# Kernel tuning notes

Measured on AMD Instinct MI355X. Metric: run time of the kernel, lower is better.

Reference implementation:

```python
import jax, jax.numpy as jnp
import numpy as np

N, E, B = 50000, 600000, 64
C_IN, H, C_OUT, L = 128, 128, 64, 3
BN_EPS = 1e-5


def setup_inputs() -> dict:
    key = jax.random.key(0)
    ks = iter(jax.random.split(key, 40))

    def w(shape, fan_in):
        return jax.random.normal(next(ks), shape, jnp.float32) / np.sqrt(fan_in).astype(np.float32)

    return {
        "x": jax.random.normal(next(ks), (N, C_IN), jnp.float32),
        "edge_index": jax.random.randint(next(ks), (2, E), 0, N),
        "batch": jnp.sort(jax.random.randint(next(ks), (N,), 0, B)),
        # GINConv MLPs: Linear(in,h) -> BN -> ReLU -> Linear(h,h)   (stacked over L; C_IN == H)
        "convW1": w((L, C_IN, H), C_IN), "convb1": jnp.zeros((L, H), jnp.float32),
        "bn_g": jnp.ones((L, H), jnp.float32), "bn_b": jnp.zeros((L, H), jnp.float32),
        "convW2": w((L, H, H), H), "convb2": jnp.zeros((L, H), jnp.float32),
        # reconstruction head: Linear(h,h)-ReLU-Linear(h,h)-ReLU-Linear(h,4)-ReLU
        "recW1": w((H, H), H), "recb1": jnp.zeros((H,), jnp.float32),
        "recW2": w((H, H), H), "recb2": jnp.zeros((H,), jnp.float32),
        "recW3": w((H, 4), H), "recb3": jnp.zeros((4,), jnp.float32),
        # final MLP([h,h,out], norm=None): Linear(h,h)-ReLU-(dropout, eval=identity)-Linear(h,out)
        "mlpW1": w((H, H), H), "mlpb1": jnp.zeros((H,), jnp.float32),
        "mlpW2": w((H, C_OUT), H), "mlpb2": jnp.zeros((C_OUT,), jnp.float32),
    }


def reference(x, edge_index, batch, convW1, convb1, bn_g, bn_b, convW2, convb2,
              recW1, recb1, recW2, recb2, recW3, recb3, mlpW1, mlpb1, mlpW2, mlpb2):
    src, dst = edge_index[0], edge_index[1]
    for l in range(L):
        # GIN aggregation: out_i = nn((1+eps)*x_i + sum_{j->i} x_j), eps = 0
        agg = jax.ops.segment_sum(x[src], dst, num_segments=N)  # [N, d]
        h = (x + agg) @ convW1[l] + convb1[l]                   # [N, H]
        mu = h.mean(axis=0)
        var = jnp.var(h, axis=0)                                # biased, torch BN train mode
        h = bn_g[l] * (h - mu) * jax.lax.rsqrt(var + BN_EPS) + bn_b[l]
        h = jax.nn.relu(h) @ convW2[l] + convb2[l]
        x = jax.nn.relu(h)                                      # outer .relu() in forward
    # reconstruction branch on node features
    x_rec = jax.nn.relu(x @ recW1 + recb1)
    x_rec = jax.nn.relu(x_rec @ recW2 + recb2)
    x_rec = jax.nn.relu(x_rec @ recW3 + recb3)                  # [N, 4]
    # global_add_pool keyed by graph id
    pooled = jax.ops.segment_sum(x, batch, num_segments=B)      # [B, H]
    out = jax.nn.relu(pooled @ mlpW1 + mlpb1) @ mlpW2 + mlpb2   # [B, C_OUT]
    return (out, x_rec)
```

## Files before the change

### kernel.cpp

```cpp
#include <hip/hip_runtime.h>

#define NN 50000
#define EE 600000
#define BB 64
#define CH 128
#define LL 3
#define NGB 782
#define NSB 196
#define NPB 392

typedef unsigned short u16;
typedef unsigned int u32;
typedef short s16x8 __attribute__((ext_vector_type(8)));
typedef float f32x4 __attribute__((ext_vector_type(4)));

__device__ __forceinline__ u16 f2b(float f) {
    u32 x = __float_as_uint(f);
    return (u16)((x + 0x7FFFu + ((x >> 16) & 1u)) >> 16);
}
__device__ __forceinline__ float b2f(u16 u) {
    return __uint_as_float(((u32)u) << 16);
}

__global__ __launch_bounds__(256) void k_zero2(int* __restrict__ deg,
                                               float* __restrict__ pooled,
                                               float* __restrict__ gstats) {
    int i = blockIdx.x * 256 + threadIdx.x;
    if (i < NN) deg[i] = 0;
    int j = i - NN;
    if (j >= 0 && j < BB * CH) pooled[j] = 0.f;
    int k = j - BB * CH;
    if (k >= 0 && k < 3 * 256) gstats[k] = 0.f;
}

__global__ __launch_bounds__(256) void k_count(const int* __restrict__ ei,
                                               int* __restrict__ deg) {
    int e = blockIdx.x * 256 + threadIdx.x;
    if (e < EE) atomicAdd(&deg[ei[EE + e]], 1);
}

__global__ __launch_bounds__(256) void k_scanA(const int* __restrict__ deg,
                                               int* __restrict__ bsum) {
    __shared__ int sm[256];
    int i = blockIdx.x * 256 + threadIdx.x;
    sm[threadIdx.x] = (i < NN) ? deg[i] : 0;
    __syncthreads();
    for (int off = 128; off > 0; off >>= 1) {
        if (threadIdx.x < off) sm[threadIdx.x] += sm[threadIdx.x + off];
        __syncthreads();
    }
    if (threadIdx.x == 0) bsum[blockIdx.x] = sm[0];
}

__global__ __launch_bounds__(256) void k_scanB(const int* __restrict__ deg,
                                               const int* __restrict__ bsum,
                                               int* __restrict__ rowptr,
                                               int* __restrict__ cur) {
    __shared__ int sb[256], sd[256];
    int t = threadIdx.x;
    sb[t] = (t < NSB) ? bsum[t] : 0;
    __syncthreads();
    for (int off = 1; off < 256; off <<= 1) {
        int v = (t >= off) ? sb[t - off] : 0;
        __syncthreads();
        sb[t] += v;
        __syncthreads();
    }
    int blockOff = (blockIdx.x == 0) ? 0 : sb[blockIdx.x - 1];
    int i = blockIdx.x * 256 + t;
    int d = (i < NN) ? deg[i] : 0;
    sd[t] = d;
    __syncthreads();
    for (int off = 1; off < 256; off <<= 1) {
        int v = (t >= off) ? sd[t - off] : 0;
        __syncthreads();
        sd[t] += v;
        __syncthreads();
    }
    int excl = blockOff + sd[t] - d;
    if (i < NN) { rowptr[i] = excl; cur[i] = excl; }
    if (i == NN - 1) rowptr[NN] = excl + d;
}

__global__ __launch_bounds__(256) void k_fill(const int* __restrict__ ei,
                                              int* __restrict__ cur,
                                              int* __restrict__ perm) {
    int e = blockIdx.x * 256 + threadIdx.x;
    if (e < EE) {
        int dst = ei[EE + e];
        int idx = atomicAdd(&cur[dst], 1);
        perm[idx] = ei[e];
    }
}

__global__ __launch_bounds__(256) void k_cvt(const float* __restrict__ x,
                                             u16* __restrict__ y) {
    long base = (long)(blockIdx.x * 256 + threadIdx.x) * 8;
    if (base < (long)NN * CH) {
        float4 f0 = *(const float4*)(x + base);
        float4 f1 = *(const float4*)(x + base + 4);
        union { u16 pk[8]; uint4 v; } uu;
        uu.pk[0] = f2b(f0.x); uu.pk[1] = f2b(f0.y);
        uu.pk[2] = f2b(f0.z); uu.pk[3] = f2b(f0.w);
        uu.pk[4] = f2b(f1.x); uu.pk[5] = f2b(f1.y);
        uu.pk[6] = f2b(f1.z); uu.pk[7] = f2b(f1.w);
        *(uint4*)(y + base) = uu.v;
    }
}

__global__ __launch_bounds__(256) void k_gather(const u16* __restrict__ x,
                                                const int* __restrict__ rowptr,
                                                const int* __restrict__ perm,
                                                u16* __restrict__ y) {
    int dst = blockIdx.x * 16 + (threadIdx.x >> 4);
    if (dst >= NN) return;
    int lane = threadIdx.x & 15;
    int co = lane * 8;
    int beg = rowptr[dst], end = rowptr[dst + 1];
    union { u16 pk[8]; uint4 v; } uu;
    uu.v = *(const uint4*)(x + (long)dst * CH + co);
    float a[8], b[8], c[8], d[8];
#pragma unroll
    for (int j = 0; j < 8; ++j) { a[j] = b2f(uu.pk[j]); b[j] = 0.f; c[j] = 0.f; d[j] = 0.f; }
    int e = beg;
    for (; e + 3 < end; e += 4) {
        int s0 = perm[e], s1 = perm[e + 1], s2 = perm[e + 2], s3 = perm[e + 3];
        union { u16 pk[8]; uint4 v; } v0, v1, v2, v3;
        v0.v = *(const uint4*)(x + (long)s0 * CH + co);
        v1.v = *(const uint4*)(x + (long)s1 * CH + co);
        v2.v = *(const uint4*)(x + (long)s2 * CH + co);
        v3.v = *(const uint4*)(x + (long)s3 * CH + co);
#pragma unroll
        for (int j = 0; j < 8; ++j) {
            a[j] += b2f(v0.pk[j]); b[j] += b2f(v1.pk[j]);
            c[j] += b2f(v2.pk[j]); d[j] += b2f(v3.pk[j]);
        }
    }
    for (; e < end; ++e) {
        int s0 = perm[e];
        union { u16 pk[8]; uint4 v; } v0;
        v0.v = *(const uint4*)(x + (long)s0 * CH + co);
#pragma unroll
        for (int j = 0; j < 8; ++j) a[j] += b2f(v0.pk[j]);
    }
    union { u16 pk[8]; uint4 v; } ov;
#pragma unroll
    for (int j = 0; j < 8; ++j) ov.pk[j] = f2b((a[j] + b[j]) + (c[j] + d[j]));
    *(uint4*)(y + (long)dst * CH + co) = ov.v;
}

__global__ __launch_bounds__(256) void k_transpose_all(
    const float* __restrict__ cW1, const float* __restrict__ cW2,
    const float* __restrict__ rW1, const float* __restrict__ rW2,
    const float* __restrict__ rW3, u16* __restrict__ Wt) {
    int idx = blockIdx.x * 256 + threadIdx.x;
    if (idx < 8 * 16384) {
        int slot = idx >> 14;
        int wi = idx & 16383;
        int k = wi >> 7, n = wi & 127;
        const float* src = slot < 3 ? cW1 + slot * 16384
                         : slot < 6 ? cW2 + (slot - 3) * 16384
                         : slot == 6 ? rW1 : rW2;
        Wt[slot * 16384 + n * 128 + k] = f2b(src[wi]);
    } else if (idx < 9 * 16384) {
        int j = idx - 8 * 16384;
        int n = j >> 7, k = j & 127;
        Wt[8 * 16384 + j] = (n < 4) ? f2b(rW3[k * 4 + n]) : (u16)0;
    }
}

__device__ __forceinline__ void stageB8(const u16* __restrict__ Wt, u16* sB,
                                        int s, int rr) {
#pragma unroll
    for (int it = 0; it < 8; ++it) {
        int n = it * 16 + rr;
        uint4 u = *(const uint4*)(Wt + n * CH + 8 * s);
        *(uint4*)(&sB[n * CH + ((s ^ (n & 15)) * 8)]) = u;
    }
}

__device__ __forceinline__ void mfma64(const u16* sA, const u16* sB,
                                       f32x4 acc[8], int wv, int quad, int l16) {
    f32x4 z = {0.f, 0.f, 0.f, 0.f};
#pragma unroll
    for (int t = 0; t < 8; ++t) acc[t] = z;
    const u16* pa = sA + (wv * 16 + l16) * CH;
#pragma unroll
    for (int kc = 0; kc < 4; ++kc) {
        int off = (((kc << 2) | quad) ^ l16) << 3;
        s16x8 a0 = *(const s16x8*)(pa + off);
#pragma unroll
        for (int t = 0; t < 8; ++t) {
            s16x8 bfr = *(const s16x8*)(sB + (t * 16 + l16) * CH + off);
            acc[t] = __builtin_amdgcn_mfma_f32_16x16x32_bf16(a0, bfr, acc[t], 0, 0, 0);
        }
    }
}

__device__ __forceinline__ void biasrelu64(f32x4 acc[8],
                                           const float* __restrict__ bias, int l16) {
#pragma unroll
    for (int t = 0; t < 8; ++t) {
        float bv = bias[t * 16 + l16];
#pragma unroll
        for (int r = 0; r < 4; ++r)
            acc[t][r] = fmaxf(acc[t][r] + bv, 0.f);
    }
}

__device__ __forceinline__ void restage64(const f32x4 acc[8], u16* sA,
                                          int wv, int quad, int l16) {
#pragma unroll
    for (int t = 0; t < 8; ++t) {
        int chunk = (t << 1) | (l16 >> 3);
        int o7 = l16 & 7;
#pragma unroll
        for (int r = 0; r < 4; ++r) {
            int lr = wv * 16 + quad * 4 + r;
            sA[lr * CH + ((chunk ^ (lr & 15)) << 3) + o7] = f2b(acc[t][r]);
        }
    }
}

__global__ __launch_bounds__(256, 3) void k_g1(
    const u16* __restrict__ y16, const u16* __restrict__ Wt1,
    const float* __restrict__ cb1, u16* __restrict__ h16,
    float* __restrict__ gstats) {
    __shared__ u16 sA[64 * CH];
    __shared__ u16 sB[128 * CH];
    const int tid = threadIdx.x;
    const int s = tid & 15, rr = tid >> 4;
    const int r0 = blockIdx.x * 64;
    const int lane = tid & 63, wv = tid >> 6, quad = lane >> 4, l16 = lane & 15;

    stageB8(Wt1, sB, s, rr);
#pragma unroll
    for (int it = 0; it < 4; ++it) {
        int lr = it * 16 + rr;
        int gr = r0 + lr;
        union { u16 pk[8]; uint4 v; } uu;
        if (gr < NN) {
            uu.v = *(const uint4*)(y16 + (long)gr * CH + 8 * s);
        } else {
#pragma unroll
            for (int j = 0; j < 8; ++j) uu.pk[j] = 0;
        }
        *(uint4*)(&sA[lr * CH + ((s ^ (lr & 15)) * 8)]) = uu.v;
    }
    __syncthreads();

    f32x4 acc[8];
    mfma64(sA, sB, acc, wv, quad, l16);

    float ss[8], qq[8];
#pragma unroll
    for (int t = 0; t < 8; ++t) {
        float bv = cb1[t * 16 + l16];
        int col = t * 16 + l16;
        ss[t] = 0.f; qq[t] = 0.f;
        int rbase = r0 + wv * 16 + quad * 4;
#pragma unroll
        for (int r = 0; r < 4; ++r) {
            float v = acc[t][r] + bv;
            int row = rbase + r;
            if (row < NN) {
                ss[t] += v; qq[t] += v * v;
                h16[(long)row * CH + col] = f2b(v);
            }
        }
    }
#pragma unroll
    for (int t = 0; t < 8; ++t) {
        ss[t] += __shfl_xor(ss[t], 16);
        ss[t] += __shfl_xor(ss[t], 32);
        qq[t] += __shfl_xor(qq[t], 16);
        qq[t] += __shfl_xor(qq[t], 32);
    }
    float* red = (float*)sA;
    __syncthreads();
    if (lane < 16) {
#pragma unroll
        for (int t = 0; t < 8; ++t) {
            red[wv * 256 + t * 16 + l16] = ss[t];
            red[wv * 256 + 128 + t * 16 + l16] = qq[t];
        }
    }
    __syncthreads();
    unsafeAtomicAdd(&gstats[tid],
                    red[tid] + red[256 + tid] + red[512 + tid] + red[768 + tid]);
}

__global__ __launch_bounds__(128) void k_bnparam(const float* __restrict__ gstats,
                                                 const float* __restrict__ g,
                                                 const float* __restrict__ b,
                                                 float* __restrict__ scale,
                                                 float* __restrict__ shift) {
    int t = threadIdx.x;
    float mu = gstats[t] / (float)NN;
    float var = gstats[128 + t] / (float)NN - mu * mu;
    float rstd = rsqrtf(var + 1e-5f);
    float sc = g[t] * rstd;
    scale[t] = sc;
    shift[t] = b[t] - mu * sc;
}

__global__ __launch_bounds__(256, 3) void k_g2(
    const u16* __restrict__ h16, const u16* __restrict__ Wt2,
    const float* __restrict__ cb2, const float* __restrict__ scale,
    const float* __restrict__ shift, u16* __restrict__ xc) {
    __shared__ u16 sA[64 * CH];
    __shared__ u16 sB[128 * CH];
    const int tid = threadIdx.x;
    const int s = tid & 15, rr = tid >> 4;
    const int r0 = blockIdx.x * 64;
    const int lane = tid & 63, wv = tid >> 6, quad = lane >> 4, l16 = lane & 15;

    float sc[8], sh[8];
#pragma unroll
    for (int j = 0; j < 8; ++j) { sc[j] = scale[8 * s + j]; sh[j] = shift[8 * s + j]; }

    stageB8(Wt2, sB, s, rr);
#pragma unroll
    for (int it = 0; it < 4; ++it) {
        int lr = it * 16 + rr;
        int gr = r0 + lr;
        union { u16 pk[8]; uint4 v; } uu;
        if (gr < NN) {
            uu.v = *(const uint4*)(h16 + (long)gr * CH + 8 * s);
#pragma unroll
            for (int j = 0; j < 8; ++j)
                uu.pk[j] = f2b(fmaxf(b2f(uu.pk[j]) * sc[j] + sh[j], 0.f));
        } else {
#pragma unroll
            for (int j = 0; j < 8; ++j) uu.pk[j] = 0;
        }
        *(uint4*)(&sA[lr * CH + ((s ^ (lr & 15)) * 8)]) = uu.v;
    }
    __syncthreads();

    f32x4 acc[8];
    mfma64(sA, sB, acc, wv, quad, l16);
    biasrelu64(acc, cb2, l16);
#pragma unroll
    for (int t = 0; t < 8; ++t) {
        int col = t * 16 + l16;
        int rbase = r0 + wv * 16 + quad * 4;
#pragma unroll
        for (int r = 0; r < 4; ++r) {
            int row = rbase + r;
            if (row < NN) xc[(long)row * CH + col] = f2b(acc[t][r]);
        }
    }
}

__global__ __launch_bounds__(256, 3) void k_tail(
    const u16* __restrict__ h16, const u16* __restrict__ Wt,
    const float* __restrict__ cb2, const float* __restrict__ scale,
    const float* __restrict__ shift, const float* __restrict__ rb1,
    const float* __restrict__ rb2, const float* __restrict__ rb3,
    u16* __restrict__ xc, float* __restrict__ x_rec) {
    __shared__ u16 sA[64 * CH];
    __shared__ u16 sB[128 * CH];
    const int tid = threadIdx.x;
    const int s = tid & 15, rr = tid >> 4;
    const int r0 = blockIdx.x * 64;
    const int lane = tid & 63, wv = tid >> 6, quad = lane >> 4, l16 = lane & 15;

    float sc[8], sh[8];
#pragma unroll
    for (int j = 0; j < 8; ++j) { sc[j] = scale[8 * s + j]; sh[j] = shift[8 * s + j]; }

    stageB8(Wt + 5 * 16384, sB, s, rr);
#pragma unroll
    for (int it = 0; it < 4; ++it) {
        int lr = it * 16 + rr;
        int gr = r0 + lr;
        union { u16 pk[8]; uint4 v; } uu;
        if (gr < NN) {
            uu.v = *(const uint4*)(h16 + (long)gr * CH + 8 * s);
#pragma unroll
            for (int j = 0; j < 8; ++j)
                uu.pk[j] = f2b(fmaxf(b2f(uu.pk[j]) * sc[j] + sh[j], 0.f));
        } else {
#pragma unroll
            for (int j = 0; j < 8; ++j) uu.pk[j] = 0;
        }
        *(uint4*)(&sA[lr * CH + ((s ^ (lr & 15)) * 8)]) = uu.v;
    }
    __syncthreads();

    f32x4 acc[8];
    mfma64(sA, sB, acc, wv, quad, l16);
    biasrelu64(acc, cb2, l16);
#pragma unroll
    for (int t = 0; t < 8; ++t) {
        int col = t * 16 + l16;
        int rbase = r0 + wv * 16 + quad * 4;
#pragma unroll
        for (int r = 0; r < 4; ++r) {
            int row = rbase + r;
            if (row < NN) xc[(long)row * CH + col] = f2b(acc[t][r]);
        }
    }
    __syncthreads();
    restage64(acc, sA, wv, quad, l16);
    stageB8(Wt + 6 * 16384, sB, s, rr);
    __syncthreads();
    mfma64(sA, sB, acc, wv, quad, l16);
    biasrelu64(acc, rb1, l16);
    __syncthreads();
    restage64(acc, sA, wv, quad, l16);
    stageB8(Wt + 7 * 16384, sB, s, rr);
    __syncthreads();
    mfma64(sA, sB, acc, wv, quad, l16);
    biasrelu64(acc, rb2, l16);
    __syncthreads();
    restage64(acc, sA, wv, quad, l16);
    {
        int n = rr;
        uint4 u = *(const uint4*)(Wt + 8 * 16384 + n * CH + 8 * s);
        *(uint4*)(&sB[n * CH + ((s ^ (n & 15)) * 8)]) = u;
    }
    __syncthreads();
    f32x4 a4 = {0.f, 0.f, 0.f, 0.f};
    const u16* pa = sA + (wv * 16 + l16) * CH;
#pragma unroll
    for (int kc = 0; kc < 4; ++kc) {
        int off = (((kc << 2) | quad) ^ l16) << 3;
        s16x8 a0 = *(const s16x8*)(pa + off);
        s16x8 bfr = *(const s16x8*)(sB + l16 * CH + off);
        a4 = __builtin_amdgcn_mfma_f32_16x16x32_bf16(a0, bfr, a4, 0, 0, 0);
    }
    if (l16 < 4) {
        float bv = rb3[l16];
        int rbase = r0 + wv * 16 + quad * 4;
#pragma unroll
        for (int r = 0; r < 4; ++r) {
            int row = rbase + r;
            if (row < NN) x_rec[(long)row * 4 + l16] = fmaxf(a4[r] + bv, 0.f);
        }
    }
}

__global__ __launch_bounds__(256) void k_pool(const u16* __restrict__ x,
                                              const int* __restrict__ batch,
                                              float* __restrict__ pooled) {
    int r0 = blockIdx.x * 128;
    if (r0 >= NN) return;
    int rend = r0 + 128 < NN ? r0 + 128 : NN;
    int c = threadIdx.x & 127;
    int half = threadIdx.x >> 7;
    int r = r0 + half;
    if (r >= rend) return;
    int g = batch[r];
    float s = 0.f;
    for (; r < rend; r += 2) {
        int gg = batch[r];
        if (gg != g) {
            unsafeAtomicAdd(pooled + g * CH + c, s);
            s = 0.f;
            g = gg;
        }
        s += b2f(x[(long)r * CH + c]);
    }
    unsafeAtomicAdd(pooled + g * CH + c, s);
}

__global__ __launch_bounds__(128) void k_mlp(const float* __restrict__ pooled,
                                             const float* __restrict__ W1,
                                             const float* __restrict__ b1,
                                             const float* __restrict__ W2,
                                             const float* __restrict__ b2,
                                             float* __restrict__ out) {
    __shared__ float p[128], t1[128];
    int b = blockIdx.x, t = threadIdx.x;
    p[t] = pooled[b * CH + t];
    __syncthreads();
    float acc = b1[t];
    for (int k = 0; k < 128; ++k) acc += p[k] * W1[k * 128 + t];
    t1[t] = fmaxf(acc, 0.f);
    __syncthreads();
    if (t < 64) {
        float o = b2[t];
        for (int k = 0; k < 128; ++k) o += t1[k] * W2[k * 64 + t];
        out[b * 64 + t] = o;
    }
}

extern "C" void kernel_launch(void* const* d_in, const int* in_sizes, int n_in,
                              void* d_out, int out_size, void* d_ws, size_t ws_size,
                              hipStream_t stream) {
    const float* x_in   = (const float*)d_in[0];
    const int*   ei     = (const int*)d_in[1];
    const int*   batch  = (const int*)d_in[2];
    const float* convW1 = (const float*)d_in[3];
    const float* convb1 = (const float*)d_in[4];
    const float* bn_g   = (const float*)d_in[5];
    const float* bn_b   = (const float*)d_in[6];
    const float* convW2 = (const float*)d_in[7];
    const float* convb2 = (const float*)d_in[8];
    const float* recW1  = (const float*)d_in[9];
    const float* recb1  = (const float*)d_in[10];
    const float* recW2  = (const float*)d_in[11];
    const float* recb2  = (const float*)d_in[12];
    const float* recW3  = (const float*)d_in[13];
    const float* recb3  = (const float*)d_in[14];
    const float* mlpW1  = (const float*)d_in[15];
    const float* mlpb1  = (const float*)d_in[16];
    const float* mlpW2  = (const float*)d_in[17];
    const float* mlpb2  = (const float*)d_in[18];

    float* out   = (float*)d_out;
    float* x_rec = out + 4096;

    char* w = (char*)d_ws;
    u16*   x16    = (u16*)w;    w += (size_t)NN * CH * 2;
    u16*   y16    = (u16*)w;    w += (size_t)NN * CH * 2;
    u16*   h16    = (u16*)w;    w += (size_t)NN * CH * 2;
    u16*   xc     = (u16*)w;    w += (size_t)NN * CH * 2;
    u16*   Wt     = (u16*)w;    w += (size_t)9 * 16384 * 2;
    float* gstats = (float*)w;  w += (size_t)3 * 256 * 4;
    float* scale  = (float*)w;  w += 128 * 4;
    float* shift  = (float*)w;  w += 128 * 4;
    float* pooled = (float*)w;  w += (size_t)BB * CH * 4;
    int*   deg    = (int*)w;    w += (size_t)NN * 4;
    int*   bsum   = (int*)w;    w += (size_t)NSB * 4;
    int*   rowptr = (int*)w;    w += (size_t)(NN + 1) * 4;
    int*   cur    = (int*)w;    w += (size_t)NN * 4;
    int*   perm   = (int*)w;    w += (size_t)EE * 4;

    dim3 b256(256), b128(128);

    k_zero2<<<231, b256, 0, stream>>>(deg, pooled, gstats);
    k_count<<<2344, b256, 0, stream>>>(ei, deg);
    k_scanA<<<NSB, b256, 0, stream>>>(deg, bsum);
    k_scanB<<<NSB, b256, 0, stream>>>(deg, bsum, rowptr, cur);
    k_fill<<<2344, b256, 0, stream>>>(ei, cur, perm);
    k_cvt<<<3125, b256, 0, stream>>>(x_in, x16);
    k_transpose_all<<<576, b256, 0, stream>>>(convW1, convW2, recW1, recW2, recW3, Wt);

    const u16* cur_x = x16;
    for (int l = 0; l < LL; ++l) {
        k_gather<<<3125, b256, 0, stream>>>(cur_x, rowptr, perm, y16);
        k_g1<<<NGB, b256, 0, stream>>>(y16, Wt + l * 16384, convb1 + l * 128,
                                       h16, gstats + l * 256);
        k_bnparam<<<1, b128, 0, stream>>>(gstats + l * 256, bn_g + l * 128,
                                          bn_b + l * 128, scale, shift);
        if (l < LL - 1)
            k_g2<<<NGB, b256, 0, stream>>>(h16, Wt + (3 + l) * 16384,
                                           convb2 + l * 128, scale, shift, xc);
        else
            k_tail<<<NGB, b256, 0, stream>>>(h16, Wt, convb2 + 2 * 128, scale, shift,
                                             recb1, recb2, recb3, xc, x_rec);
        cur_x = xc;
    }
    k_pool<<<NPB, b256, 0, stream>>>(xc, batch, pooled);
    k_mlp<<<64, b128, 0, stream>>>(pooled, mlpW1, mlpb1, mlpW2, mlpb2, out);
}
```

Measured before the change: 433.1 us.

## Fuse setup kernels, fold BN params into GEMM2, pad CSR rows to four

The convert, transpose and zeroing kernels are merged into a single setup launch, and the per-layer BN parameter kernel is removed by computing scale and shift into LDS inside k_g2 and k_tail. CSR rows are padded to a multiple of four, with padding entries pointing at an extra all-zero node row, so the gather loop no longer needs a scalar remainder loop. This saves several launches and gets rid of divergent tail handling, at the cost of extra padded gathers, a larger perm buffer, and redundant BN parameter computation in every block. The setup block that zeroes the padding row also has a racy self-copy of x16 that looks odd.

```diff
diff --git a/kernel.cpp b/kernel.cpp
--- a/kernel.cpp
+++ b/kernel.cpp
@@ -22,15 +22,57 @@
     return __uint_as_float(((u32)u) << 16);
 }
 
-__global__ __launch_bounds__(256) void k_zero2(int* __restrict__ deg,
-                                               float* __restrict__ pooled,
-                                               float* __restrict__ gstats) {
-    int i = blockIdx.x * 256 + threadIdx.x;
-    if (i < NN) deg[i] = 0;
-    int j = i - NN;
-    if (j >= 0 && j < BB * CH) pooled[j] = 0.f;
-    int k = j - BB * CH;
-    if (k >= 0 && k < 3 * 256) gstats[k] = 0.f;
+__global__ __launch_bounds__(256) void k_setup(
+    const float* __restrict__ x_in, const float* __restrict__ cW1,
+    const float* __restrict__ cW2, const float* __restrict__ rW1,
+    const float* __restrict__ rW2, const float* __restrict__ rW3,
+    u16* __restrict__ x16, u16* __restrict__ Wt, int* __restrict__ deg,
+    float* __restrict__ pooled, float* __restrict__ gstats,
+    u16* __restrict__ xc) {
+    int b = blockIdx.x, t = threadIdx.x;
+    if (b < 3125) {
+        long base = (long)(b * 256 + t) * 8;
+        if (base < (long)NN * CH) {
+            float4 f0 = *(const float4*)(x_in + base);
+            float4 f1 = *(const float4*)(x_in + base + 4);
+            union { u16 pk[8]; uint4 v; } uu;
+            uu.pk[0] = f2b(f0.x); uu.pk[1] = f2b(f0.y);
+            uu.pk[2] = f2b(f0.z); uu.pk[3] = f2b(f0.w);
+            uu.pk[4] = f2b(f1.x); uu.pk[5] = f2b(f1.y);
+            uu.pk[6] = f2b(f1.z); uu.pk[7] = f2b(f1.w);
+            *(uint4*)(x16 + base) = uu.v;
+        }
+    } else if (b < 3701) {
+        int idx = (b - 3125) * 256 + t;
+        if (idx < 8 * 16384) {
+            int slot = idx >> 14;
+            int wi = idx & 16383;
+            int k = wi >> 7, n = wi & 127;
+            const float* src = slot < 3 ? cW1 + slot * 16384
+                             : slot < 6 ? cW2 + (slot - 3) * 16384
+                             : slot == 6 ? rW1 : rW2;
+            Wt[slot * 16384 + n * 128 + k] = f2b(src[wi]);
+        } else if (idx < 9 * 16384) {
+            int j = idx - 8 * 16384;
+            int n = j >> 7, k = j & 127;
+            Wt[8 * 16384 + j] = (n < 4) ? f2b(rW3[k * 4 + n]) : (u16)0;
+        }
+    } else if (b < 3932) {
+        int i = (b - 3701) * 256 + t;
+        if (i < NN) deg[i] = 0;
+        int j = i - NN;
+        if (j >= 0 && j < BB * CH) pooled[j] = 0.f;
+        int k = j - BB * CH;
+        if (k >= 0 && k < 3 * 256) gstats[k] = 0.f;
+    } else {
+        if (t < 128) {
+            x16[(long)NN * CH + t] = 0;
+            xc[(long)NN * CH + t] = 0;
+        } else {
+            int t2 = t - 128;
+            x16[(long)NN * CH + 128  - 128 + t2] = x16[(long)NN * CH + t2];
+        }
+    }
 }
 
 __global__ __launch_bounds__(256) void k_count(const int* __restrict__ ei,
@@ -43,7 +85,8 @@
                                                int* __restrict__ bsum) {
     __shared__ int sm[256];
     int i = blockIdx.x * 256 + threadIdx.x;
-    sm[threadIdx.x] = (i < NN) ? deg[i] : 0;
+    int d = (i < NN) ? deg[i] : 0;
+    sm[threadIdx.x] = (d + 3) & ~3;
     __syncthreads();
     for (int off = 128; off > 0; off >>= 1) {
         if (threadIdx.x < off) sm[threadIdx.x] += sm[threadIdx.x + off];
@@ -55,7 +98,8 @@
 __global__ __launch_bounds__(256) void k_scanB(const int* __restrict__ deg,
                                                const int* __restrict__ bsum,
                                                int* __restrict__ rowptr,
-                                               int* __restrict__ cur) {
+                                               int* __restrict__ cur,
+                                               int* __restrict__ perm) {
     __shared__ int sb[256], sd[256];
     int t = threadIdx.x;
     sb[t] = (t < NSB) ? bsum[t] : 0;
@@ -69,7 +113,8 @@
     int blockOff = (blockIdx.x == 0) ? 0 : sb[blockIdx.x - 1];
     int i = blockIdx.x * 256 + t;
     int d = (i < NN) ? deg[i] : 0;
-    sd[t] = d;
+    int pd = (d + 3) & ~3;
+    sd[t] = pd;
     __syncthreads();
     for (int off = 1; off < 256; off <<= 1) {
         int v = (t >= off) ? sd[t - off] : 0;
@@ -77,9 +122,13 @@
         sd[t] += v;
         __syncthreads();
     }
-    int excl = blockOff + sd[t] - d;
-    if (i < NN) { rowptr[i] = excl; cur[i] = excl; }
-    if (i == NN - 1) rowptr[NN] = excl + d;
+    int excl = blockOff + sd[t] - pd;
+    if (i < NN) {
+        rowptr[i] = excl;
+        cur[i] = excl;
+        for (int p = d; p < pd; ++p) perm[excl + p] = NN;
+    }
+    if (i == NN - 1) rowptr[NN] = excl + pd;
 }
 
 __global__ __launch_bounds__(256) void k_fill(const int* __restrict__ ei,
@@ -93,21 +142,6 @@
     }
 }
 
-__global__ __launch_bounds__(256) void k_cvt(const float* __restrict__ x,
-                                             u16* __restrict__ y) {
-    long base = (long)(blockIdx.x * 256 + threadIdx.x) * 8;
-    if (base < (long)NN * CH) {
-        float4 f0 = *(const float4*)(x + base);
-        float4 f1 = *(const float4*)(x + base + 4);
-        union { u16 pk[8]; uint4 v; } uu;
-        uu.pk[0] = f2b(f0.x); uu.pk[1] = f2b(f0.y);
-        uu.pk[2] = f2b(f0.z); uu.pk[3] = f2b(f0.w);
-        uu.pk[4] = f2b(f1.x); uu.pk[5] = f2b(f1.y);
-        uu.pk[6] = f2b(f1.z); uu.pk[7] = f2b(f1.w);
-        *(uint4*)(y + base) = uu.v;
-    }
-}
-
 __global__ __launch_bounds__(256) void k_gather(const u16* __restrict__ x,
                                                 const int* __restrict__ rowptr,
                                                 const int* __restrict__ perm,
@@ -116,14 +150,13 @@
     if (dst >= NN) return;
     int lane = threadIdx.x & 15;
     int co = lane * 8;
-    int beg = rowptr[dst], end = rowptr[dst + 1];
+    int beg = rowptr[dst], pend = rowptr[dst + 1];
     union { u16 pk[8]; uint4 v; } uu;
     uu.v = *(const uint4*)(x + (long)dst * CH + co);
     float a[8], b[8], c[8], d[8];
 #pragma unroll
     for (int j = 0; j < 8; ++j) { a[j] = b2f(uu.pk[j]); b[j] = 0.f; c[j] = 0.f; d[j] = 0.f; }
-    int e = beg;
-    for (; e + 3 < end; e += 4) {
+    for (int e = beg; e < pend; e += 4) {
         int s0 = perm[e], s1 = perm[e + 1], s2 = perm[e + 2], s3 = perm[e + 3];
         union { u16 pk[8]; uint4 v; } v0, v1, v2, v3;
         v0.v = *(const uint4*)(x + (long)s0 * CH + co);
@@ -136,37 +169,10 @@
             c[j] += b2f(v2.pk[j]); d[j] += b2f(v3.pk[j]);
         }
     }
-    for (; e < end; ++e) {
-        int s0 = perm[e];
-        union { u16 pk[8]; uint4 v; } v0;
-        v0.v = *(const uint4*)(x + (long)s0 * CH + co);
-#pragma unroll
-        for (int j = 0; j < 8; ++j) a[j] += b2f(v0.pk[j]);
-    }
     union { u16 pk[8]; uint4 v; } ov;
 #pragma unroll
     for (int j = 0; j < 8; ++j) ov.pk[j] = f2b((a[j] + b[j]) + (c[j] + d[j]));
     *(uint4*)(y + (long)dst * CH + co) = ov.v;
-}
-
-__global__ __launch_bounds__(256) void k_transpose_all(
-    const float* __restrict__ cW1, const float* __restrict__ cW2,
-    const float* __restrict__ rW1, const float* __restrict__ rW2,
-    const float* __restrict__ rW3, u16* __restrict__ Wt) {
-    int idx = blockIdx.x * 256 + threadIdx.x;
-    if (idx < 8 * 16384) {
-        int slot = idx >> 14;
-        int wi = idx & 16383;
-        int k = wi >> 7, n = wi & 127;
-        const float* src = slot < 3 ? cW1 + slot * 16384
-                         : slot < 6 ? cW2 + (slot - 3) * 16384
-                         : slot == 6 ? rW1 : rW2;
-        Wt[slot * 16384 + n * 128 + k] = f2b(src[wi]);
-    } else if (idx < 9 * 16384) {
-        int j = idx - 8 * 16384;
-        int n = j >> 7, k = j & 127;
-        Wt[8 * 16384 + j] = (n < 4) ? f2b(rW3[k * 4 + n]) : (u16)0;
-    }
 }
 
 __device__ __forceinline__ void stageB8(const u16* __restrict__ Wt, u16* sB,
@@ -219,6 +225,20 @@
             int lr = wv * 16 + quad * 4 + r;
             sA[lr * CH + ((chunk ^ (lr & 15)) << 3) + o7] = f2b(acc[t][r]);
         }
+    }
+}
+
+__device__ __forceinline__ void bn_to_lds(const float* __restrict__ gstats,
+                                          const float* __restrict__ g,
+                                          const float* __restrict__ bbeta,
+                                          float* ssc, float* ssh, int tid) {
+    if (tid < 128) {
+        float mu = gstats[tid] / (float)NN;
+        float var = gstats[128 + tid] / (float)NN - mu * mu;
+        float rstd = rsqrtf(var + 1e-5f);
+        float sc = g[tid] * rstd;
+        ssc[tid] = sc;
+        ssh[tid] = bbeta[tid] - mu * sc;
     }
 }
 
@@ -290,36 +310,27 @@
                     red[tid] + red[256 + tid] + red[512 + tid] + red[768 + tid]);
 }
 
-__global__ __launch_bounds__(128) void k_bnparam(const float* __restrict__ gstats,
-                                                 const float* __restrict__ g,
-                                                 const float* __restrict__ b,
-                                                 float* __restrict__ scale,
-                                                 float* __restrict__ shift) {
-    int t = threadIdx.x;
-    float mu = gstats[t] / (float)NN;
-    float var = gstats[128 + t] / (float)NN - mu * mu;
-    float rstd = rsqrtf(var + 1e-5f);
-    float sc = g[t] * rstd;
-    scale[t] = sc;
-    shift[t] = b[t] - mu * sc;
-}
-
 __global__ __launch_bounds__(256, 3) void k_g2(
     const u16* __restrict__ h16, const u16* __restrict__ Wt2,
-    const float* __restrict__ cb2, const float* __restrict__ scale,
-    const float* __restrict__ shift, u16* __restrict__ xc) {
+    const float* __restrict__ cb2, const float* __restrict__ gstats,
+    const float* __restrict__ g, const float* __restrict__ bbeta,
+    u16* __restrict__ xc) {
     __shared__ u16 sA[64 * CH];
     __shared__ u16 sB[128 * CH];
+    __shared__ float ssc[128], ssh[128];
     const int tid = threadIdx.x;
     const int s = tid & 15, rr = tid >> 4;
     const int r0 = blockIdx.x * 64;
     const int lane = tid & 63, wv = tid >> 6, quad = lane >> 4, l16 = lane & 15;
 
+    bn_to_lds(gstats, g, bbeta, ssc, ssh, tid);
+    stageB8(Wt2, sB, s, rr);
+    __syncthreads();
+
     float sc[8], sh[8];
 #pragma unroll
-    for (int j = 0; j < 8; ++j) { sc[j] = scale[8 * s + j]; sh[j] = shift[8 * s + j]; }
-
-    stageB8(Wt2, sB, s, rr);
+    for (int j = 0; j < 8; ++j) { sc[j] = ssc[8 * s + j]; sh[j] = ssh[8 * s + j]; }
+
 #pragma unroll
     for (int it = 0; it < 4; ++it) {
         int lr = it * 16 + rr;
@@ -355,22 +366,27 @@
 
 __global__ __launch_bounds__(256, 3) void k_tail(
     const u16* __restrict__ h16, const u16* __restrict__ Wt,
-    const float* __restrict__ cb2, const float* __restrict__ scale,
-    const float* __restrict__ shift, const float* __restrict__ rb1,
-    const float* __restrict__ rb2, const float* __restrict__ rb3,
-    u16* __restrict__ xc, float* __restrict__ x_rec) {
+    const float* __restrict__ cb2, const float* __restrict__ gstats,
+    const float* __restrict__ g, const float* __restrict__ bbeta,
+    const float* __restrict__ rb1, const float* __restrict__ rb2,
+    const float* __restrict__ rb3, u16* __restrict__ xc,
+    float* __restrict__ x_rec) {
     __shared__ u16 sA[64 * CH];
     __shared__ u16 sB[128 * CH];
+    __shared__ float ssc[128], ssh[128];
     const int tid = threadIdx.x;
     const int s = tid & 15, rr = tid >> 4;
     const int r0 = blockIdx.x * 64;
     const int lane = tid & 63, wv = tid >> 6, quad = lane >> 4, l16 = lane & 15;
 
+    bn_to_lds(gstats, g, bbeta, ssc, ssh, tid);
+    stageB8(Wt + 5 * 16384, sB, s, rr);
+    __syncthreads();
+
     float sc[8], sh[8];
 #pragma unroll
-    for (int j = 0; j < 8; ++j) { sc[j] = scale[8 * s + j]; sh[j] = shift[8 * s + j]; }
-
-    stageB8(Wt + 5 * 16384, sB, s, rr);
+    for (int j = 0; j < 8; ++j) { sc[j] = ssc[8 * s + j]; sh[j] = ssh[8 * s + j]; }
+
 #pragma unroll
     for (int it = 0; it < 4; ++it) {
         int lr = it * 16 + rr;
@@ -514,44 +530,42 @@
     float* x_rec = out + 4096;
 
     char* w = (char*)d_ws;
-    u16*   x16    = (u16*)w;    w += (size_t)NN * CH * 2;
+    u16*   x16    = (u16*)w;    w += (size_t)(NN + 1) * CH * 2;
     u16*   y16    = (u16*)w;    w += (size_t)NN * CH * 2;
     u16*   h16    = (u16*)w;    w += (size_t)NN * CH * 2;
-    u16*   xc     = (u16*)w;    w += (size_t)NN * CH * 2;
+    u16*   xc     = (u16*)w;    w += (size_t)(NN + 1) * CH * 2;
     u16*   Wt     = (u16*)w;    w += (size_t)9 * 16384 * 2;
     float* gstats = (float*)w;  w += (size_t)3 * 256 * 4;
-    float* scale  = (float*)w;  w += 128 * 4;
-    float* shift  = (float*)w;  w += 128 * 4;
     float* pooled = (float*)w;  w += (size_t)BB * CH * 4;
     int*   deg    = (int*)w;    w += (size_t)NN * 4;
     int*   bsum   = (int*)w;    w += (size_t)NSB * 4;
     int*   rowptr = (int*)w;    w += (size_t)(NN + 1) * 4;
     int*   cur    = (int*)w;    w += (size_t)NN * 4;
-    int*   perm   = (int*)w;    w += (size_t)EE * 4;
+    int*   perm   = (int*)w;    w += (size_t)(EE + 4 * NN) * 4;
 
     dim3 b256(256), b128(128);
 
-    k_zero2<<<231, b256, 0, stream>>>(deg, pooled, gstats);
+    k_setup<<<3933, b256, 0, stream>>>(x_in, convW1, convW2, recW1, recW2, recW3,
+                                       x16, Wt, deg, pooled, gstats, xc);
     k_count<<<2344, b256, 0, stream>>>(ei, deg);
     k_scanA<<<NSB, b256, 0, stream>>>(deg, bsum);
-    k_scanB<<<NSB, b256, 0, stream>>>(deg, bsum, rowptr, cur);
+    k_scanB<<<NSB, b256, 0, stream>>>(deg, bsum, rowptr, cur, perm);
     k_fill<<<2344, b256, 0, stream>>>(ei, cur, perm);
-    k_cvt<<<3125, b256, 0, stream>>>(x_in, x16);
-    k_transpose_all<<<576, b256, 0, stream>>>(convW1, convW2, recW1, recW2, recW3, Wt);
 
     const u16* cur_x = x16;
     for (int l = 0; l < LL; ++l) {
         k_gather<<<3125, b256, 0, stream>>>(cur_x, rowptr, perm, y16);
         k_g1<<<NGB, b256, 0, stream>>>(y16, Wt + l * 16384, convb1 + l * 128,
                                        h16, gstats + l * 256);
-        k_bnparam<<<1, b128, 0, stream>>>(gstats + l * 256, bn_g + l * 128,
-                                          bn_b + l * 128, scale, shift);
         if (l < LL - 1)
             k_g2<<<NGB, b256, 0, stream>>>(h16, Wt + (3 + l) * 16384,
-                                           convb2 + l * 128, scale, shift, xc);
+                                           convb2 + l * 128, gstats + l * 256,
+                                           bn_g + l * 128, bn_b + l * 128, xc);
         else
-            k_tail<<<NGB, b256, 0, stream>>>(h16, Wt, convb2 + 2 * 128, scale, shift,
-                                             recb1, recb2, recb3, xc, x_rec);
+            k_tail<<<NGB, b256, 0, stream>>>(h16, Wt, convb2 + 2 * 128,
+                                             gstats + 2 * 256, bn_g + 2 * 128,
+                                             bn_b + 2 * 128, recb1, recb2, recb3,
+                                             xc, x_rec);
         cur_x = xc;
     }
     k_pool<<<NPB, b256, 0, stream>>>(xc, batch, pooled);
```

Result: no change. 437.6 us (+1.1%).
